# Optimization experiments

Measured on AMD Instinct MI355X. Metric: run time of the kernel, lower is better.

The kernel has to match this reference:

```python
import jax, jax.numpy as jnp
import numpy as np

N = 100000
E = 1600000
C = 64   # in_channels == out_channels
D = 3    # pos dim
H = 64   # pos_nn / attn_nn hidden width


def _mlp2(x, W1, b1, W2, b2):
    # PyG MLP([a, h, c], plain_last=False, act='relu'): Linear->(BN)->ReLU twice.
    # BatchNorm in eval mode with default running stats (mean=0, var=1) is ~identity
    # and is omitted here.
    h = jax.nn.relu(x @ W1 + b1)
    return jax.nn.relu(h @ W2 + b2)


def setup_inputs() -> dict:
    key = jax.random.key(0)
    ks = jax.random.split(key, 20)
    x = jax.random.normal(ks[0], (N, C), dtype=jnp.float32)
    pos = jax.random.normal(ks[1], (N, D), dtype=jnp.float32)
    # edges with no self loops (module asserts this; conv adds its own)
    src = jax.random.randint(ks[2], (E,), 0, N)
    off = jax.random.randint(ks[3], (E,), 1, N)
    dst = (src + off) % N
    edge_index = jnp.stack([src, dst]).astype(jnp.int64)

    def lin(k, fi, fo):
        return jax.random.normal(k, (fo, fi), dtype=jnp.float32) / np.sqrt(fi)

    return {
        "x": x, "pos": pos, "edge_index": edge_index,
        "W_in": lin(ks[4], C, C), "b_in": jnp.zeros((C,), jnp.float32),
        "W_out": lin(ks[5], C, C), "b_out": jnp.zeros((C,), jnp.float32),
        # PointTransformerConv internal linears (bias=False)
        "W_lin": lin(ks[6], C, C),
        "W_src": lin(ks[7], C, C),
        "W_dst": lin(ks[8], C, C),
        # pos_nn: [D, H, C]
        "pW1": lin(ks[9], D, H).T, "pb1": jnp.zeros((H,), jnp.float32),
        "pW2": lin(ks[10], H, C).T, "pb2": jnp.zeros((C,), jnp.float32),
        # attn_nn: [C, H, C]
        "aW1": lin(ks[11], C, H).T, "ab1": jnp.zeros((H,), jnp.float32),
        "aW2": lin(ks[12], H, C).T, "ab2": jnp.zeros((C,), jnp.float32),
    }


def reference(x, pos, edge_index, W_in, b_in, W_out, b_out, W_lin, W_src, W_dst,
              pW1, pb1, pW2, pb2, aW1, ab1, aW2, ab2):
    n = x.shape[0]
    x = jax.nn.relu(x @ W_in.T + b_in)

    # PointTransformerConv: per-node projections
    alpha_src = x @ W_src.T   # alpha_j source term
    alpha_dst = x @ W_dst.T   # alpha_i target term
    xv = x @ W_lin.T          # value projection

    # add self loops
    loops = jnp.arange(n, dtype=edge_index.dtype)
    src = jnp.concatenate([edge_index[0], loops])
    dst = jnp.concatenate([edge_index[1], loops])

    # message: delta = pos_nn(pos_i - pos_j); alpha = attn_nn(a_i - a_j + delta)
    delta = _mlp2(pos[dst] - pos[src], pW1, pb1, pW2, pb2)          # [E', C]
    a = _mlp2(alpha_dst[dst] - alpha_src[src] + delta, aW1, ab1, aW2, ab2)

    # softmax over edges grouped by destination node
    amax = jax.ops.segment_max(a, dst, num_segments=n)
    e = jnp.exp(a - amax[dst])
    esum = jax.ops.segment_sum(e, dst, num_segments=n)
    w = e / esum[dst]

    msg = w * (xv[src] + delta)
    out = jax.ops.segment_max(msg, dst, num_segments=n)  # aggr='max'; self-loops => no empty segments

    return jax.nn.relu(out @ W_out.T + b_out)
```

## Files before the change

### kernel.cpp

```cpp
#include <hip/hip_runtime.h>
#include <hip/hip_bf16.h>

#define CC 64

typedef __attribute__((ext_vector_type(8))) short s16x8;
typedef __attribute__((ext_vector_type(4))) float f32x4;

__device__ __forceinline__ unsigned short f2b(float f) {
    unsigned u = __float_as_uint(f);
    u += 0x7FFF + ((u >> 16) & 1);
    return (unsigned short)(u >> 16);
}
__device__ __forceinline__ float b2f(unsigned short b) {
    return __uint_as_float((unsigned)b << 16);
}
__device__ __forceinline__ unsigned fmono(float f) {
    unsigned u = __float_as_uint(f);
    return u ^ ((unsigned)((int)u >> 31) | 0x80000000u);
}

__global__ __launch_bounds__(256, 2) void node_mfma_kernel(
    const float* __restrict__ x,
    const float* __restrict__ W_in, const float* __restrict__ b_in,
    const float* __restrict__ W_src, const float* __restrict__ W_dst,
    const float* __restrict__ W_lin, const float* __restrict__ aW1,
    unsigned short* __restrict__ ASb, unsigned short* __restrict__ ADb,
    unsigned short* __restrict__ xvb,
    const int* __restrict__ ei, unsigned* __restrict__ cnt, int N, int E)
{
    const int tid = threadIdx.x;
    const int lane = tid & 63;
    const int wid  = tid >> 6;
    const int lm = lane & 15;
    const int lg = lane >> 4;

    __shared__ __align__(16) unsigned short swt[5][64 * 72];
    __shared__ __align__(16) unsigned short tb[4][16 * 72];

    {
        const float* Wr[4] = {W_in, W_src, W_dst, W_lin};
        #pragma unroll
        for (int w = 0; w < 4; ++w)
            for (int idx = tid; idx < 4096; idx += 256) {
                int o = idx >> 6, k = idx & 63;
                swt[w][o*72 + k] = f2b(Wr[w][(size_t)o*64 + k]);
            }
        for (int idx = tid; idx < 4096; idx += 256) {
            int k = idx >> 6, o = idx & 63;
            swt[4][o*72 + k] = f2b(aW1[idx]);
        }
    }
    __syncthreads();

    const int wbase = blockIdx.x * 64 + wid * 16;
    unsigned short* tbw = tb[wid];

    if (wbase < N) {
        float bin[4];
        #pragma unroll
        for (int tt = 0; tt < 4; ++tt) bin[tt] = b_in[lm + 16*tt];

        const int xrow = min(wbase + lm, N-1);
        const float* xp = &x[(size_t)xrow*CC];
        float4 a0 = *(const float4*)&xp[lg*8];
        float4 a1 = *(const float4*)&xp[lg*8 + 4];
        float4 a2 = *(const float4*)&xp[32 + lg*8];
        float4 a3 = *(const float4*)&xp[32 + lg*8 + 4];
        s16x8 Xlo, Xhi;
        Xlo[0]=(short)f2b(a0.x); Xlo[1]=(short)f2b(a0.y); Xlo[2]=(short)f2b(a0.z); Xlo[3]=(short)f2b(a0.w);
        Xlo[4]=(short)f2b(a1.x); Xlo[5]=(short)f2b(a1.y); Xlo[6]=(short)f2b(a1.z); Xlo[7]=(short)f2b(a1.w);
        Xhi[0]=(short)f2b(a2.x); Xhi[1]=(short)f2b(a2.y); Xhi[2]=(short)f2b(a2.z); Xhi[3]=(short)f2b(a2.w);
        Xhi[4]=(short)f2b(a3.x); Xhi[5]=(short)f2b(a3.y); Xhi[6]=(short)f2b(a3.z); Xhi[7]=(short)f2b(a3.w);

        auto mm = [&](s16x8 alo, s16x8 ahi, int w, f32x4* zz) {
            #pragma unroll
            for (int tt = 0; tt < 4; ++tt) {
                s16x8 b0 = *(const s16x8*)&swt[w][(lm + 16*tt)*72 + lg*8];
                s16x8 b1 = *(const s16x8*)&swt[w][(lm + 16*tt)*72 + 32 + lg*8];
                f32x4 z = {0.f, 0.f, 0.f, 0.f};
                z = __builtin_amdgcn_mfma_f32_16x16x32_bf16(alo, b0, z, 0, 0, 0);
                zz[tt] = __builtin_amdgcn_mfma_f32_16x16x32_bf16(ahi, b1, z, 0, 0, 0);
            }
        };
        auto transpose = [&](const f32x4* zz, s16x8& olo, s16x8& ohi) {
            #pragma unroll
            for (int tt = 0; tt < 4; ++tt)
                #pragma unroll
                for (int r = 0; r < 4; ++r)
                    tbw[(lg*4+r)*72 + lm + 16*tt] = f2b(zz[tt][r]);
            __builtin_amdgcn_wave_barrier();
            olo = *(const s16x8*)&tbw[lm*72 + lg*8];
            ohi = *(const s16x8*)&tbw[lm*72 + 32 + lg*8];
            __builtin_amdgcn_wave_barrier();
        };
        auto store_perm = [&](const f32x4* zz, unsigned short* out) {
            #pragma unroll
            for (int r = 0; r < 4; ++r) {
                int n = wbase + lg*4 + r;
                if (n < N) {
                    ushort4 v = make_ushort4(f2b(zz[0][r]), f2b(zz[1][r]),
                                             f2b(zz[2][r]), f2b(zz[3][r]));
                    *(ushort4*)&out[(size_t)n*CC + lm*4] = v;
                }
            }
        };

        f32x4 zh[4], zt[4], zo[4];
        mm(Xlo, Xhi, 0, zh);
        #pragma unroll
        for (int tt = 0; tt < 4; ++tt)
            #pragma unroll
            for (int r = 0; r < 4; ++r)
                zh[tt][r] = fmaxf(zh[tt][r] + bin[tt], 0.f);
        s16x8 Hlo, Hhi;
        transpose(zh, Hlo, Hhi);

        mm(Hlo, Hhi, 1, zt);
        { s16x8 Tlo, Thi; transpose(zt, Tlo, Thi); mm(Tlo, Thi, 4, zo); }
        store_perm(zo, ASb);

        mm(Hlo, Hhi, 2, zt);
        { s16x8 Tlo, Thi; transpose(zt, Tlo, Thi); mm(Tlo, Thi, 4, zo); }
        store_perm(zo, ADb);

        mm(Hlo, Hhi, 3, zo);
        store_perm(zo, xvb);
    }

    const int total = E + N;
    for (int e = blockIdx.x*256 + tid; e < total; e += gridDim.x*256) {
        int d = (e < E) ? min(max(ei[(size_t)E + e], 0), N-1) : (e - E);
        atomicAdd(&cnt[d], 1u);
    }
}

#define SCAN_T 256
__global__ __launch_bounds__(SCAN_T) void scan1_kernel(
    const unsigned* __restrict__ cnt, unsigned* __restrict__ chunk_off,
    unsigned* __restrict__ partials, int n)
{
    __shared__ unsigned sh[SCAN_T];
    const int t = threadIdx.x, b0 = blockIdx.x * (SCAN_T*4);
    unsigned v[4], s = 0;
    #pragma unroll
    for (int i = 0; i < 4; ++i) {
        int idx = b0 + t*4 + i;
        v[i] = (idx < n) ? cnt[idx] : 0u;
        s += v[i];
    }
    sh[t] = s; __syncthreads();
    for (int d = 1; d < SCAN_T; d <<= 1) {
        unsigned xv = (t >= d) ? sh[t-d] : 0u;
        __syncthreads();
        sh[t] += xv;
        __syncthreads();
    }
    unsigned run = (t > 0) ? sh[t-1] : 0u;
    #pragma unroll
    for (int i = 0; i < 4; ++i) {
        int idx = b0 + t*4 + i;
        if (idx < n) chunk_off[idx] = run;
        run += v[i];
    }
    if (t == SCAN_T-1) partials[blockIdx.x] = sh[SCAN_T-1];
}

__global__ __launch_bounds__(1024) void scan2_kernel(unsigned* __restrict__ partials, int nb)
{
    __shared__ unsigned sh[1024];
    const int t = threadIdx.x;
    sh[t] = (t < nb) ? partials[t] : 0u; __syncthreads();
    for (int d = 1; d < 1024; d <<= 1) {
        unsigned xv = (t >= d) ? sh[t-d] : 0u;
        __syncthreads();
        sh[t] += xv;
        __syncthreads();
    }
    if (t < nb) partials[t] = (t > 0) ? sh[t-1] : 0u;
}

__global__ __launch_bounds__(256) void scan3_kernel(
    const unsigned* __restrict__ chunk_off, const unsigned* __restrict__ partials,
    unsigned* __restrict__ cursor, int n)
{
    int i = blockIdx.x*256 + threadIdx.x;
    if (i < n) cursor[i] = chunk_off[i] + partials[i >> 10];
}

__global__ __launch_bounds__(256) void scatter_kernel(
    const int* __restrict__ ei, unsigned* __restrict__ cursor,
    int2* __restrict__ rec, int N, int E)
{
    const int total = E + N;
    for (int e = blockIdx.x*256 + threadIdx.x; e < total; e += gridDim.x*256) {
        int s, d;
        if (e < E) {
            s = min(max(ei[e], 0), N-1);
            d = min(max(ei[(size_t)E + e], 0), N-1);
        } else { s = d = e - E; }
        unsigned p = atomicAdd(&cursor[d], 1u);
        rec[p] = make_int2(s, d);
    }
}

__global__ __launch_bounds__(256, 3) void edge_mfma_kernel(
    const int2* __restrict__ rec, const float* __restrict__ pos,
    const unsigned short* __restrict__ ADb, const unsigned short* __restrict__ ASb,
    const unsigned short* __restrict__ xvb,
    const float* __restrict__ pW1, const float* __restrict__ pb1,
    const float* __restrict__ pW2, const float* __restrict__ pb2,
    const float* __restrict__ aW1, const float* __restrict__ ab1,
    const float* __restrict__ aW2, const float* __restrict__ ab2,
    float* __restrict__ esum, unsigned* __restrict__ outb,
    int N, int E)
{
    const int tid = threadIdx.x;
    const int lane = tid & 63;
    const int wid  = tid >> 6;
    const int lm = lane & 15;
    const int lg = lane >> 4;

    __shared__ __align__(16) unsigned short swt[3][64 * 72];
    __shared__ __align__(16) unsigned short tb[4][16 * 72];
    __shared__ unsigned spw[2][64];

    {
        const float* Wsrc[3] = {pW2, aW1, aW2};
        #pragma unroll
        for (int w = 0; w < 3; ++w)
            for (int idx = tid; idx < 4096; idx += 256) {
                int k = idx >> 6, o = idx & 63;
                swt[w][o*72 + k] = f2b(Wsrc[w][idx]);
            }
        if (tid < 64) {
            spw[0][tid] = (unsigned)f2b(pW1[tid])     | ((unsigned)f2b(pW1[64+tid]) << 16);
            spw[1][tid] = (unsigned)f2b(pW1[128+tid]) | ((unsigned)f2b(pb1[tid])    << 16);
        }
    }
    __syncthreads();

    float pb2v[4], ab1v[4], ab2v[4];
    #pragma unroll
    for (int tt = 0; tt < 4; ++tt) {
        pb2v[tt] = pb2[lm + 16*tt];
        ab1v[tt] = ab1[lm + 16*tt];
        ab2v[tt] = ab2[lm + 16*tt];
    }

    unsigned short* tbw = tb[wid];
    const int total = E + N;
    const int ntiles = (total + 15) >> 4;
    const int nwaves = gridDim.x * 4;
    const int tpw = (ntiles + nwaves - 1) / nwaves;
    const int gw = blockIdx.x * 4 + wid;
    const int t0 = min(gw * tpw, ntiles);
    const int t1 = min(t0 + tpw, ntiles);
    if (t0 >= t1) return;
    const int nstep = t1 - t0;
    const int qlen  = 4 * nstep;
    const int rbase = t0 << 4;
    const int pq = rbase + (lm >> 2)*qlen + (lm & 3);
    const int gq = rbase + lg*qlen;

    int   curD = -1;
    bool  firstF = true;
    float sA[4]  = {0.f, 0.f, 0.f, 0.f};
    float mxA[4] = {-INFINITY, -INFINITY, -INFINITY, -INFINITY};

    int2 rp_n, rg_n0, rg_n1, rg_n2, rg_n3;
    rp_n  = rec[min(pq, total-1)];
    rg_n0 = rec[min(gq+0, total-1)];
    rg_n1 = rec[min(gq+1, total-1)];
    rg_n2 = rec[min(gq+2, total-1)];
    rg_n3 = rec[min(gq+3, total-1)];

    for (int step = 0; step < nstep; ++step) {
        const int2 rp = rp_n;
        int sg[4], dg[4];
        sg[0] = rg_n0.x; dg[0] = rg_n0.y;
        sg[1] = rg_n1.x; dg[1] = rg_n1.y;
        sg[2] = rg_n2.x; dg[2] = rg_n2.y;
        sg[3] = rg_n3.x; dg[3] = rg_n3.y;
        int actm = 0;
        #pragma unroll
        for (int r = 0; r < 4; ++r)
            if (gq + step*4 + r < total) actm |= (1 << r);

        float q0 = pos[(size_t)rp.y*3+0] - pos[(size_t)rp.x*3+0];
        float q1 = pos[(size_t)rp.y*3+1] - pos[(size_t)rp.x*3+1];
        float q2 = pos[(size_t)rp.y*3+2] - pos[(size_t)rp.x*3+2];

        float gd[4][4], gxv[4][4];
        #pragma unroll
        for (int r = 0; r < 4; ++r) {
            const ushort4 a4 = *(const ushort4*)&ADb[(size_t)dg[r]*CC + lm*4];
            const ushort4 s4 = *(const ushort4*)&ASb[(size_t)sg[r]*CC + lm*4];
            const ushort4 x4 = *(const ushort4*)&xvb[(size_t)sg[r]*CC + lm*4];
            gd[r][0] = b2f(a4.x) - b2f(s4.x);
            gd[r][1] = b2f(a4.y) - b2f(s4.y);
            gd[r][2] = b2f(a4.z) - b2f(s4.z);
            gd[r][3] = b2f(a4.w) - b2f(s4.w);
            gxv[r][0] = b2f(x4.x); gxv[r][1] = b2f(x4.y);
            gxv[r][2] = b2f(x4.z); gxv[r][3] = b2f(x4.w);
        }

        if (step + 1 < nstep) {
            const int pn = pq + (step+1)*4;
            const int gn = gq + (step+1)*4;
            rp_n  = rec[min(pn,   total-1)];
            rg_n0 = rec[min(gn+0, total-1)];
            rg_n1 = rec[min(gn+1, total-1)];
            rg_n2 = rec[min(gn+2, total-1)];
            rg_n3 = rec[min(gn+3, total-1)];
        }

        s16x8 Alo, Ahi;
        #pragma unroll
        for (int j = 0; j < 16; ++j) {
            int k = lg*8 + (j & 7) + 32*(j >> 3);
            unsigned wa = ((volatile unsigned*)spw[0])[k];
            unsigned wb = ((volatile unsigned*)spw[1])[k];
            float w0 = __uint_as_float(wa << 16);
            float w1 = __uint_as_float(wa & 0xFFFF0000u);
            float w2 = __uint_as_float(wb << 16);
            float bb = __uint_as_float(wb & 0xFFFF0000u);
            float v = fmaxf(fmaf(q0, w0, fmaf(q1, w1, fmaf(q2, w2, bb))), 0.f);
            short b = (short)f2b(v);
            if (j < 8) Alo[j] = b; else Ahi[j-8] = b;
        }

        f32x4 dlt[4];
        #pragma unroll
        for (int tt = 0; tt < 4; ++tt) {
            s16x8 b0 = *(const s16x8*)&swt[0][(lm + 16*tt)*72 + lg*8];
            s16x8 b1 = *(const s16x8*)&swt[0][(lm + 16*tt)*72 + 32 + lg*8];
            f32x4 z = {0.f, 0.f, 0.f, 0.f};
            z = __builtin_amdgcn_mfma_f32_16x16x32_bf16(Alo, b0, z, 0, 0, 0);
            z = __builtin_amdgcn_mfma_f32_16x16x32_bf16(Ahi, b1, z, 0, 0, 0);
            #pragma unroll
            for (int r = 0; r < 4; ++r) dlt[tt][r] = fmaxf(z[r] + pb2v[tt], 0.f);
        }

        #pragma unroll
        for (int tt = 0; tt < 4; ++tt)
            #pragma unroll
            for (int r = 0; r < 4; ++r)
                tbw[(lg*4+r)*72 + lm + 16*tt] = f2b(dlt[tt][r]);
        __builtin_amdgcn_wave_barrier();
        s16x8 Dlo = *(const s16x8*)&tbw[lm*72 + lg*8];
        s16x8 Dhi = *(const s16x8*)&tbw[lm*72 + 32 + lg*8];
        __builtin_amdgcn_wave_barrier();

        #pragma unroll
        for (int tt = 0; tt < 4; ++tt) {
            s16x8 b0 = *(const s16x8*)&swt[1][(lm + 16*tt)*72 + lg*8];
            s16x8 b1 = *(const s16x8*)&swt[1][(lm + 16*tt)*72 + 32 + lg*8];
            f32x4 z = {0.f, 0.f, 0.f, 0.f};
            z = __builtin_amdgcn_mfma_f32_16x16x32_bf16(Dlo, b0, z, 0, 0, 0);
            z = __builtin_amdgcn_mfma_f32_16x16x32_bf16(Dhi, b1, z, 0, 0, 0);
            #pragma unroll
            for (int r = 0; r < 4; ++r) {
                float v = fmaxf(z[r] + gd[r][tt] + ab1v[tt], 0.f);
                tbw[(lg*4+r)*72 + lm + 16*tt] = f2b(v);
            }
        }
        __builtin_amdgcn_wave_barrier();
        s16x8 Hlo = *(const s16x8*)&tbw[lm*72 + lg*8];
        s16x8 Hhi = *(const s16x8*)&tbw[lm*72 + 32 + lg*8];
        __builtin_amdgcn_wave_barrier();

        f32x4 zz[4];
        #pragma unroll
        for (int tt = 0; tt < 4; ++tt) {
            s16x8 b0 = *(const s16x8*)&swt[2][(lm + 16*tt)*72 + lg*8];
            s16x8 b1 = *(const s16x8*)&swt[2][(lm + 16*tt)*72 + 32 + lg*8];
            f32x4 z = {0.f, 0.f, 0.f, 0.f};
            z = __builtin_amdgcn_mfma_f32_16x16x32_bf16(Hlo, b0, z, 0, 0, 0);
            zz[tt] = __builtin_amdgcn_mfma_f32_16x16x32_bf16(Hhi, b1, z, 0, 0, 0);
        }

        #pragma unroll
        for (int r = 0; r < 4; ++r) {
            if (!(actm & (1 << r))) continue;
            if (dg[r] != curD) {
                if (curD >= 0) {
                    if (firstF) {
                        #pragma unroll
                        for (int tt = 0; tt < 4; ++tt) {
                            size_t off = (size_t)curD*CC + lm + 16*tt;
                            atomicAdd(&esum[off], sA[tt]);
                            atomicMax(&outb[off], fmono(mxA[tt]));
                        }
                    } else {
                        #pragma unroll
                        for (int tt = 0; tt < 4; ++tt) {
                            size_t off = (size_t)curD*CC + lm + 16*tt;
                            esum[off] = sA[tt];
                            outb[off] = fmono(mxA[tt]);
                        }
                    }
                    firstF = false;
                }
                curD = dg[r];
                #pragma unroll
                for (int tt = 0; tt < 4; ++tt) { sA[tt] = 0.f; mxA[tt] = -INFINITY; }
            }
            #pragma unroll
            for (int tt = 0; tt < 4; ++tt) {
                float a  = fmaxf(zz[tt][r] + ab2v[tt], 0.f);
                float ee = __expf(a);
                float m  = ee * (gxv[r][tt] + dlt[tt][r]);
                sA[tt] += ee;
                mxA[tt] = fmaxf(mxA[tt], m);
            }
        }
    }

    if (curD >= 0) {
        #pragma unroll
        for (int tt = 0; tt < 4; ++tt) {
            size_t off = (size_t)curD*CC + lm + 16*tt;
            atomicAdd(&esum[off], sA[tt]);
            atomicMax(&outb[off], fmono(mxA[tt]));
        }
    }
}

__global__ __launch_bounds__(256, 2) void out_kernel(
    const unsigned* outb_in,
    const float* __restrict__ esum,
    const float* __restrict__ W_out, const float* __restrict__ b_out,
    float* out, int N)
{
    __shared__ float vt[64][68];
    const int t = threadIdx.x, lane = t & 63, quad = t >> 6;
    const int n0 = blockIdx.x * 64;
    float wreg[64];
    #pragma unroll
    for (int k4 = 0; k4 < 16; ++k4)
        *(float4*)&wreg[k4*4] = *(const float4*)&W_out[(size_t)lane*CC + k4*4];
    #pragma unroll 4
    for (int i = 0; i < 16; ++i) {
        int r = i*4 + quad, n = n0 + r;
        float v = 0.f;
        if (n < N) {
            unsigned u = outb_in[(size_t)n*CC + lane];
            u = (u >> 31) ? (u ^ 0x80000000u) : ~u;
            v = __uint_as_float(u) / esum[(size_t)n*CC + lane];
        }
        vt[r][lane] = v;
    }
    __syncthreads();
    const float bo = b_out[lane];
    #pragma unroll 2
    for (int i = 0; i < 16; ++i) {
        int r = i*4 + quad, n = n0 + r;
        if (n >= N) continue;
        float acc = bo;
        #pragma unroll
        for (int k4 = 0; k4 < 16; ++k4) {
            float4 xx = *(const float4*)&vt[r][k4*4];
            acc += xx.x*wreg[k4*4+0] + xx.y*wreg[k4*4+1]
                 + xx.z*wreg[k4*4+2] + xx.w*wreg[k4*4+3];
        }
        out[(size_t)n*CC + lane] = fmaxf(acc, 0.f);
    }
}

extern "C" void kernel_launch(void* const* d_in, const int* in_sizes, int n_in,
                              void* d_out, int out_size, void* d_ws, size_t ws_size,
                              hipStream_t stream)
{
    const float* x     = (const float*)d_in[0];
    const float* pos   = (const float*)d_in[1];
    const int*   ei    = (const int*)d_in[2];
    const float* W_in  = (const float*)d_in[3];
    const float* b_in  = (const float*)d_in[4];
    const float* W_out = (const float*)d_in[5];
    const float* b_out = (const float*)d_in[6];
    const float* W_lin = (const float*)d_in[7];
    const float* W_src = (const float*)d_in[8];
    const float* W_dst = (const float*)d_in[9];
    const float* pW1   = (const float*)d_in[10];
    const float* pb1   = (const float*)d_in[11];
    const float* pW2   = (const float*)d_in[12];
    const float* pb2   = (const float*)d_in[13];
    const float* aW1   = (const float*)d_in[14];
    const float* ab1   = (const float*)d_in[15];
    const float* aW2   = (const float*)d_in[16];
    const float* ab2   = (const float*)d_in[17];

    const int N = in_sizes[0] / CC;
    const int E = in_sizes[2] / 2;
    const size_t nc = (size_t)N * CC;

    char* wsb = (char*)d_ws;
    unsigned short* ASb = (unsigned short*)wsb;
    unsigned short* ADb = ASb + nc;
    unsigned short* xvb = ADb + nc;
    float* esum = (float*)(((size_t)(xvb + nc) + 15) & ~(size_t)15);
    unsigned* cnt       = (unsigned*)(esum + nc);
    unsigned* chunk_off = cnt + N;
    unsigned* cursor    = chunk_off + N;
    unsigned* partials  = cursor + N;
    size_t rec_off = ((size_t)((char*)(partials + 1024) - wsb) + 15) & ~(size_t)15;
    int2* rec = (int2*)(wsb + rec_off);
    unsigned* outb = (unsigned*)d_out;

    hipMemsetAsync(esum, 0, nc*sizeof(float), stream);
    hipMemsetAsync(outb, 0, nc*sizeof(float), stream);
    hipMemsetAsync(cnt, 0, (size_t)N*sizeof(unsigned), stream);

    const int nblk = (N + 63) / 64;
    node_mfma_kernel<<<nblk, 256, 0, stream>>>(x, W_in, b_in, W_src, W_dst, W_lin, aW1,
                                               ASb, ADb, xvb, ei, cnt, N, E);
    const int nchunks = (N + 1023) / 1024;
    scan1_kernel<<<nchunks, SCAN_T, 0, stream>>>(cnt, chunk_off, partials, N);
    scan2_kernel<<<1, 1024, 0, stream>>>(partials, nchunks);
    scan3_kernel<<<(N + 255)/256, 256, 0, stream>>>(chunk_off, partials, cursor, N);
    scatter_kernel<<<2048, 256, 0, stream>>>(ei, cursor, rec, N, E);
    edge_mfma_kernel<<<2048, 256, 0, stream>>>(rec, pos, ADb, ASb, xvb,
                                               pW1, pb1, pW2, pb2, aW1, ab1, aW2, ab2,
                                               esum, outb, N, E);
    out_kernel<<<nblk, 256, 0, stream>>>(outb, esum, W_out, b_out, (float*)d_out, N);
}
```

Before: 498.5 us.

## Port output projection to bf16 MFMA, change LDS padding, use native bf16 convert

The final output kernel, which did the W_out projection as a per-lane fp32 dot product out of LDS, is replaced by a bf16 MFMA version. Each wave now loads 16 node rows, normalises them with a fast divide, converts them to bf16 and multiplies by W_out held in LDS. The LDS row pitch for the weight and transpose tiles changes from 72 to 74 elements in all kernels, intended to reduce bank conflicts. The hand-rolled float-to-bf16 rounding is swapped for the compiler's native __bf16 conversion. The 74-element pitch (148 bytes) no longer keeps the 16-byte vector LDS reads aligned, which may split or slow those loads. The output GEMM now runs at bf16 precision.

```diff
diff --git a/kernel.cpp b/kernel.cpp
--- a/kernel.cpp
+++ b/kernel.cpp
@@ -2,14 +2,14 @@
 #include <hip/hip_bf16.h>
 
 #define CC 64
+#define WPAD 74
 
 typedef __attribute__((ext_vector_type(8))) short s16x8;
 typedef __attribute__((ext_vector_type(4))) float f32x4;
 
 __device__ __forceinline__ unsigned short f2b(float f) {
-    unsigned u = __float_as_uint(f);
-    u += 0x7FFF + ((u >> 16) & 1);
-    return (unsigned short)(u >> 16);
+    __bf16 h = (__bf16)f;
+    return __builtin_bit_cast(unsigned short, h);
 }
 __device__ __forceinline__ float b2f(unsigned short b) {
     return __uint_as_float((unsigned)b << 16);
@@ -34,8 +34,8 @@
     const int lm = lane & 15;
     const int lg = lane >> 4;
 
-    __shared__ __align__(16) unsigned short swt[5][64 * 72];
-    __shared__ __align__(16) unsigned short tb[4][16 * 72];
+    __shared__ __align__(16) unsigned short swt[5][64 * WPAD];
+    __shared__ __align__(16) unsigned short tb[4][16 * WPAD];
 
     {
         const float* Wr[4] = {W_in, W_src, W_dst, W_lin};
@@ -43,11 +43,11 @@
         for (int w = 0; w < 4; ++w)
             for (int idx = tid; idx < 4096; idx += 256) {
                 int o = idx >> 6, k = idx & 63;
-                swt[w][o*72 + k] = f2b(Wr[w][(size_t)o*64 + k]);
+                swt[w][o*WPAD + k] = f2b(Wr[w][(size_t)o*64 + k]);
             }
         for (int idx = tid; idx < 4096; idx += 256) {
             int k = idx >> 6, o = idx & 63;
-            swt[4][o*72 + k] = f2b(aW1[idx]);
+            swt[4][o*WPAD + k] = f2b(aW1[idx]);
         }
     }
     __syncthreads();
@@ -75,8 +75,8 @@
         auto mm = [&](s16x8 alo, s16x8 ahi, int w, f32x4* zz) {
             #pragma unroll
             for (int tt = 0; tt < 4; ++tt) {
-                s16x8 b0 = *(const s16x8*)&swt[w][(lm + 16*tt)*72 + lg*8];
-                s16x8 b1 = *(const s16x8*)&swt[w][(lm + 16*tt)*72 + 32 + lg*8];
+                s16x8 b0 = *(const s16x8*)&swt[w][(lm + 16*tt)*WPAD + lg*8];
+                s16x8 b1 = *(const s16x8*)&swt[w][(lm + 16*tt)*WPAD + 32 + lg*8];
                 f32x4 z = {0.f, 0.f, 0.f, 0.f};
                 z = __builtin_amdgcn_mfma_f32_16x16x32_bf16(alo, b0, z, 0, 0, 0);
                 zz[tt] = __builtin_amdgcn_mfma_f32_16x16x32_bf16(ahi, b1, z, 0, 0, 0);
@@ -87,10 +87,10 @@
             for (int tt = 0; tt < 4; ++tt)
                 #pragma unroll
                 for (int r = 0; r < 4; ++r)
-                    tbw[(lg*4+r)*72 + lm + 16*tt] = f2b(zz[tt][r]);
+                    tbw[(lg*4+r)*WPAD + lm + 16*tt] = f2b(zz[tt][r]);
             __builtin_amdgcn_wave_barrier();
-            olo = *(const s16x8*)&tbw[lm*72 + lg*8];
-            ohi = *(const s16x8*)&tbw[lm*72 + 32 + lg*8];
+            olo = *(const s16x8*)&tbw[lm*WPAD + lg*8];
+            ohi = *(const s16x8*)&tbw[lm*WPAD + 32 + lg*8];
             __builtin_amdgcn_wave_barrier();
         };
         auto store_perm = [&](const f32x4* zz, unsigned short* out) {
@@ -220,8 +220,8 @@
     const int lm = lane & 15;
     const int lg = lane >> 4;
 
-    __shared__ __align__(16) unsigned short swt[3][64 * 72];
-    __shared__ __align__(16) unsigned short tb[4][16 * 72];
+    __shared__ __align__(16) unsigned short swt[3][64 * WPAD];
+    __shared__ __align__(16) unsigned short tb[4][16 * WPAD];
     __shared__ unsigned spw[2][64];
 
     {
@@ -230,7 +230,7 @@
         for (int w = 0; w < 3; ++w)
             for (int idx = tid; idx < 4096; idx += 256) {
                 int k = idx >> 6, o = idx & 63;
-                swt[w][o*72 + k] = f2b(Wsrc[w][idx]);
+                swt[w][o*WPAD + k] = f2b(Wsrc[w][idx]);
             }
         if (tid < 64) {
             spw[0][tid] = (unsigned)f2b(pW1[tid])     | ((unsigned)f2b(pW1[64+tid]) << 16);
@@ -332,8 +332,8 @@
         f32x4 dlt[4];
         #pragma unroll
         for (int tt = 0; tt < 4; ++tt) {
-            s16x8 b0 = *(const s16x8*)&swt[0][(lm + 16*tt)*72 + lg*8];
-            s16x8 b1 = *(const s16x8*)&swt[0][(lm + 16*tt)*72 + 32 + lg*8];
+            s16x8 b0 = *(const s16x8*)&swt[0][(lm + 16*tt)*WPAD + lg*8];
+            s16x8 b1 = *(const s16x8*)&swt[0][(lm + 16*tt)*WPAD + 32 + lg*8];
             f32x4 z = {0.f, 0.f, 0.f, 0.f};
             z = __builtin_amdgcn_mfma_f32_16x16x32_bf16(Alo, b0, z, 0, 0, 0);
             z = __builtin_amdgcn_mfma_f32_16x16x32_bf16(Ahi, b1, z, 0, 0, 0);
@@ -345,35 +345,35 @@
         for (int tt = 0; tt < 4; ++tt)
             #pragma unroll
             for (int r = 0; r < 4; ++r)
-                tbw[(lg*4+r)*72 + lm + 16*tt] = f2b(dlt[tt][r]);
+                tbw[(lg*4+r)*WPAD + lm + 16*tt] = f2b(dlt[tt][r]);
         __builtin_amdgcn_wave_barrier();
-        s16x8 Dlo = *(const s16x8*)&tbw[lm*72 + lg*8];
-        s16x8 Dhi = *(const s16x8*)&tbw[lm*72 + 32 + lg*8];
+        s16x8 Dlo = *(const s16x8*)&tbw[lm*WPAD + lg*8];
+        s16x8 Dhi = *(const s16x8*)&tbw[lm*WPAD + 32 + lg*8];
         __builtin_amdgcn_wave_barrier();
 
         #pragma unroll
         for (int tt = 0; tt < 4; ++tt) {
-            s16x8 b0 = *(const s16x8*)&swt[1][(lm + 16*tt)*72 + lg*8];
-            s16x8 b1 = *(const s16x8*)&swt[1][(lm + 16*tt)*72 + 32 + lg*8];
+            s16x8 b0 = *(const s16x8*)&swt[1][(lm + 16*tt)*WPAD + lg*8];
+            s16x8 b1 = *(const s16x8*)&swt[1][(lm + 16*tt)*WPAD + 32 + lg*8];
             f32x4 z = {0.f, 0.f, 0.f, 0.f};
             z = __builtin_amdgcn_mfma_f32_16x16x32_bf16(Dlo, b0, z, 0, 0, 0);
             z = __builtin_amdgcn_mfma_f32_16x16x32_bf16(Dhi, b1, z, 0, 0, 0);
             #pragma unroll
             for (int r = 0; r < 4; ++r) {
                 float v = fmaxf(z[r] + gd[r][tt] + ab1v[tt], 0.f);
-                tbw[(lg*4+r)*72 + lm + 16*tt] = f2b(v);
+                tbw[(lg*4+r)*WPAD + lm + 16*tt] = f2b(v);
             }
         }
         __builtin_amdgcn_wave_barrier();
-        s16x8 Hlo = *(const s16x8*)&tbw[lm*72 + lg*8];
-        s16x8 Hhi = *(const s16x8*)&tbw[lm*72 + 32 + lg*8];
+        s16x8 Hlo = *(const s16x8*)&tbw[lm*WPAD + lg*8];
+        s16x8 Hhi = *(const s16x8*)&tbw[lm*WPAD + 32 + lg*8];
         __builtin_amdgcn_wave_barrier();
 
         f32x4 zz[4];
         #pragma unroll
         for (int tt = 0; tt < 4; ++tt) {
-            s16x8 b0 = *(const s16x8*)&swt[2][(lm + 16*tt)*72 + lg*8];
-            s16x8 b1 = *(const s16x8*)&swt[2][(lm + 16*tt)*72 + 32 + lg*8];
+            s16x8 b0 = *(const s16x8*)&swt[2][(lm + 16*tt)*WPAD + lg*8];
+            s16x8 b1 = *(const s16x8*)&swt[2][(lm + 16*tt)*WPAD + 32 + lg*8];
             f32x4 z = {0.f, 0.f, 0.f, 0.f};
             z = __builtin_amdgcn_mfma_f32_16x16x32_bf16(Hlo, b0, z, 0, 0, 0);
             zz[tt] = __builtin_amdgcn_mfma_f32_16x16x32_bf16(Hhi, b1, z, 0, 0, 0);
@@ -426,44 +426,71 @@
     }
 }
 
-__global__ __launch_bounds__(256, 2) void out_kernel(
+__global__ __launch_bounds__(256, 2) void out_mfma_kernel(
     const unsigned* outb_in,
     const float* __restrict__ esum,
     const float* __restrict__ W_out, const float* __restrict__ b_out,
     float* out, int N)
 {
-    __shared__ float vt[64][68];
-    const int t = threadIdx.x, lane = t & 63, quad = t >> 6;
-    const int n0 = blockIdx.x * 64;
-    float wreg[64];
-    #pragma unroll
-    for (int k4 = 0; k4 < 16; ++k4)
-        *(float4*)&wreg[k4*4] = *(const float4*)&W_out[(size_t)lane*CC + k4*4];
-    #pragma unroll 4
-    for (int i = 0; i < 16; ++i) {
-        int r = i*4 + quad, n = n0 + r;
-        float v = 0.f;
+    const int tid = threadIdx.x;
+    const int lane = tid & 63;
+    const int wid  = tid >> 6;
+    const int lm = lane & 15;
+    const int lg = lane >> 4;
+
+    __shared__ __align__(16) unsigned short swt[64 * WPAD];
+    for (int idx = tid; idx < 4096; idx += 256) {
+        int o = idx >> 6, k = idx & 63;
+        swt[o*WPAD + k] = f2b(W_out[(size_t)o*64 + k]);
+    }
+    __syncthreads();
+
+    const int wbase = blockIdx.x * 64 + wid * 16;
+    if (wbase >= N) return;
+
+    const int row = min(wbase + lm, N-1);
+    const unsigned* up = &outb_in[(size_t)row*CC];
+    const float*    ep = &esum[(size_t)row*CC];
+    s16x8 Alo, Ahi;
+    #pragma unroll
+    for (int half = 0; half < 2; ++half) {
+        int kb = half*32 + lg*8;
+        uint4  u0 = *(const uint4*)&up[kb];
+        uint4  u1 = *(const uint4*)&up[kb+4];
+        float4 e0 = *(const float4*)&ep[kb];
+        float4 e1 = *(const float4*)&ep[kb+4];
+        unsigned uu[8] = {u0.x,u0.y,u0.z,u0.w,u1.x,u1.y,u1.z,u1.w};
+        float    ee[8] = {e0.x,e0.y,e0.z,e0.w,e1.x,e1.y,e1.z,e1.w};
+        #pragma unroll
+        for (int j = 0; j < 8; ++j) {
+            unsigned u = uu[j];
+            u = (u >> 31) ? (u ^ 0x80000000u) : ~u;
+            float v = __fdividef(__uint_as_float(u), ee[j]);
+            if (half == 0) Alo[j] = (short)f2b(v); else Ahi[j] = (short)f2b(v);
+        }
+    }
+
+    f32x4 zz[4];
+    #pragma unroll
+    for (int tt = 0; tt < 4; ++tt) {
+        s16x8 b0 = *(const s16x8*)&swt[(lm + 16*tt)*WPAD + lg*8];
+        s16x8 b1 = *(const s16x8*)&swt[(lm + 16*tt)*WPAD + 32 + lg*8];
+        f32x4 z = {0.f, 0.f, 0.f, 0.f};
+        z = __builtin_amdgcn_mfma_f32_16x16x32_bf16(Alo, b0, z, 0, 0, 0);
+        zz[tt] = __builtin_amdgcn_mfma_f32_16x16x32_bf16(Ahi, b1, z, 0, 0, 0);
+    }
+    float bo[4];
+    #pragma unroll
+    for (int tt = 0; tt < 4; ++tt) bo[tt] = b_out[lm + 16*tt];
+
+    #pragma unroll
+    for (int r = 0; r < 4; ++r) {
+        int n = wbase + lg*4 + r;
         if (n < N) {
-            unsigned u = outb_in[(size_t)n*CC + lane];
-            u = (u >> 31) ? (u ^ 0x80000000u) : ~u;
-            v = __uint_as_float(u) / esum[(size_t)n*CC + lane];
-        }
-        vt[r][lane] = v;
-    }
-    __syncthreads();
-    const float bo = b_out[lane];
-    #pragma unroll 2
-    for (int i = 0; i < 16; ++i) {
-        int r = i*4 + quad, n = n0 + r;
-        if (n >= N) continue;
-        float acc = bo;
-        #pragma unroll
-        for (int k4 = 0; k4 < 16; ++k4) {
-            float4 xx = *(const float4*)&vt[r][k4*4];
-            acc += xx.x*wreg[k4*4+0] + xx.y*wreg[k4*4+1]
-                 + xx.z*wreg[k4*4+2] + xx.w*wreg[k4*4+3];
-        }
-        out[(size_t)n*CC + lane] = fmaxf(acc, 0.f);
+            #pragma unroll
+            for (int tt = 0; tt < 4; ++tt)
+                out[(size_t)n*CC + lm + 16*tt] = fmaxf(zz[tt][r] + bo[tt], 0.f);
+        }
     }
 }
 
@@ -522,5 +549,5 @@
     edge_mfma_kernel<<<2048, 256, 0, stream>>>(rec, pos, ADb, ASb, xvb,
                                                pW1, pb1, pW2, pb2, aW1, ab1, aW2, ab2,
                                                esum, outb, N, E);
-    out_kernel<<<nblk, 256, 0, stream>>>(outb, esum, W_out, b_out, (float*)d_out, N);
-}
+    out_mfma_kernel<<<nblk, 256, 0, stream>>>(outb, esum, W_out, b_out, (float*)d_out, N);
+}
```

After: 517.1 us. 1.04x slower.
